# Kernel optimization log

Measured on AMD Instinct MI355X. Metric: run time of the kernel, lower is better.

The kernel has to match this reference:

```python
import jax, jax.numpy as jnp
import numpy as np

B, K, D = 8192, 64, 128
LOW_BOUND = 1
TAU = 1.0  # global_step=None -> tau = 1.0


def setup_inputs() -> dict:
    key = jax.random.key(0)
    ks = jax.random.split(key, 7)
    slots = jax.random.normal(ks[0], (B, K, D), dtype=jnp.float32)
    gumbel_u = jax.random.uniform(ks[1], (B, K, 2), dtype=jnp.float32)
    fix_u = jax.random.uniform(ks[2], (B, K), dtype=jnp.float32)
    # score_net params: Linear(D, D//2) -> ReLU -> Linear(D//2, 2)
    H = D // 2
    W1 = jax.random.normal(ks[3], (D, H), dtype=jnp.float32) / np.sqrt(D)
    b1 = jnp.zeros((H,), dtype=jnp.float32)
    W2 = jax.random.normal(ks[4], (H, 2), dtype=jnp.float32) / np.sqrt(H)
    b2 = jnp.zeros((2,), dtype=jnp.float32)
    return {"slots": slots, "gumbel_u": gumbel_u, "fix_u": fix_u,
            "W1": W1, "b1": b1, "W2": W2, "b2": b2}


def reference(slots, gumbel_u, fix_u, W1, b1, W2, b2):
    # score_net MLP: [B,K,D] -> [B,K,2]
    h = jax.nn.relu(jnp.einsum('bkd,dh->bkh', slots, W1) + b1)
    logits = jnp.einsum('bkh,ht->bkt', h, W2) + b2

    # hard gumbel-softmax (training path), straight-through estimator
    u = jnp.clip(gumbel_u, 1e-10, 1.0 - 1e-7)
    g = -jnp.log(-jnp.log(u))
    y_soft = jax.nn.softmax((logits + g) / TAU, axis=-1)
    y_hard = jax.nn.one_hot(jnp.argmax(y_soft, axis=-1), 2, dtype=y_soft.dtype)
    y = y_hard + y_soft - jax.lax.stop_gradient(y_soft)
    decision = y[..., 1]  # [B, K]

    # vectorized _ensure_minimum_slots: activate `deficit` random inactive slots
    active = decision != 0                                   # [B, K]
    needed = jnp.maximum(LOW_BOUND - active.sum(-1), 0)[:, None]  # [B, 1]
    keys = jnp.where(active, -jnp.inf, fix_u)                # random keys on inactive slots
    ranks = jnp.argsort(jnp.argsort(-keys, axis=-1), axis=-1)  # rank 0 = largest key
    activate = (ranks < needed) & (~active)
    decision = jnp.where(activate, jnp.asarray(1.0, decision.dtype), decision)

    keep_probs = jax.nn.softmax(logits, axis=-1)[..., 1]     # [B, K]
    return decision, keep_probs
```

## Files before the change

### kernel.cpp

```cpp
#include <hip/hip_runtime.h>


typedef __attribute__((ext_vector_type(8))) short bf16x8;
typedef __attribute__((ext_vector_type(4))) float f32x4;

constexpr int NROWS = 8192 * 64;
constexpr int D = 128, H = 64;

__device__ __forceinline__ void split3(float x, unsigned& h1, unsigned& h2, unsigned& h3) {
    unsigned ux = __float_as_uint(x);
    h1 = ux & 0xFFFF0000u;
    float r = x - __uint_as_float(h1);
    h2 = __float_as_uint(r) & 0xFFFF0000u;
    float r2 = r - __uint_as_float(h2);
    h3 = __float_as_uint(r2) & 0xFFFF0000u;
}

__global__ __launch_bounds__(512, 2)
void gumbel_slot_mfma(const float* __restrict__ slots,
                      const float* __restrict__ gumbel_u,
                      const float* __restrict__ fix_u,
                      const float* __restrict__ W1,
                      const float* __restrict__ b1,
                      const float* __restrict__ W2,
                      const float* __restrict__ b2,
                      float* __restrict__ out)
{
    __shared__ __align__(16) unsigned short wt[3 * 64 * 128];
    __shared__ __align__(16) float red[8][16][16][2];

    const int tid  = threadIdx.x;
    const int wv   = tid >> 6;
    const int lane = tid & 63;
    const int quad = lane >> 4;
    const int col  = lane & 15;

#pragma unroll
    for (int i = 0; i < 16; ++i) {
        const int e = i * 512 + tid;
        const int d = e >> 6, j = e & 63;
        unsigned h1, h2, h3;
        split3(W1[e], h1, h2, h3);
        const int chunk = (d >> 3) ^ (j & 15);
        const int idx = j * 128 + chunk * 8 + (d & 7);
        wt[idx]             = (unsigned short)(h1 >> 16);
        wt[idx + 8192]      = (unsigned short)(h2 >> 16);
        wt[idx + 16384]     = (unsigned short)(h3 >> 16);
    }
    __syncthreads();

    float  b1v[4];
    float2 w2v[4];
#pragma unroll
    for (int nt = 0; nt < 4; ++nt) {
        b1v[nt] = b1[nt * 16 + col];
        w2v[nt] = *(const float2*)(W2 + (size_t)(nt * 16 + col) * 2);
    }
    const float2 b2v = *(const float2*)b2;

#pragma unroll 1
    for (int t = 0; t < 2; ++t) {
        const int tile = blockIdx.x + t * 512;
        const int rowW = tile * 512 + wv * 64;
        const int r    = rowW + lane;

        f32x4 acc[4][4];
#pragma unroll
        for (int mt = 0; mt < 4; ++mt)
#pragma unroll
            for (int nt = 0; nt < 4; ++nt)
                acc[mt][nt] = f32x4{b1v[nt], b1v[nt], b1v[nt], b1v[nt]};

#pragma unroll 1
        for (int ks = 0; ks < 4; ++ks) {
            bf16x8 a1[4], a2[4], a3[4];
#pragma unroll
            for (int mt = 0; mt < 4; ++mt) {
                const float* arow = slots + (size_t)(rowW + mt * 16 + col) * D
                                          + ks * 32 + quad * 8;
                const float4 x0 = *(const float4*)arow;
                const float4 x1 = *(const float4*)(arow + 4);
                const float xs[8] = {x0.x, x0.y, x0.z, x0.w, x1.x, x1.y, x1.z, x1.w};
                union { int i[4]; bf16x8 v; } u1, u2, u3;
#pragma unroll
                for (int p = 0; p < 4; ++p) {
                    unsigned xh1, xh2, xh3, yh1, yh2, yh3;
                    split3(xs[2 * p],     xh1, xh2, xh3);
                    split3(xs[2 * p + 1], yh1, yh2, yh3);
                    u1.i[p] = (int)((xh1 >> 16) | yh1);
                    u2.i[p] = (int)((xh2 >> 16) | yh2);
                    u3.i[p] = (int)((xh3 >> 16) | yh3);
                }
                a1[mt] = u1.v; a2[mt] = u2.v; a3[mt] = u3.v;
            }
#pragma unroll
            for (int nt = 0; nt < 4; ++nt) {
                const int j = nt * 16 + col;
                const int chunk = (ks * 4 + quad) ^ col;
                const unsigned short* wp = &wt[j * 128 + chunk * 8];
                const bf16x8 bq1 = *(const bf16x8*)(wp);
                const bf16x8 bq2 = *(const bf16x8*)(wp + 8192);
                const bf16x8 bq3 = *(const bf16x8*)(wp + 16384);
#pragma unroll
                for (int mt = 0; mt < 4; ++mt) {
                    f32x4 c = acc[mt][nt];
                    c = __builtin_amdgcn_mfma_f32_16x16x32_bf16(a1[mt], bq1, c, 0, 0, 0);
                    c = __builtin_amdgcn_mfma_f32_16x16x32_bf16(a2[mt], bq1, c, 0, 0, 0);
                    c = __builtin_amdgcn_mfma_f32_16x16x32_bf16(a1[mt], bq2, c, 0, 0, 0);
                    c = __builtin_amdgcn_mfma_f32_16x16x32_bf16(a2[mt], bq2, c, 0, 0, 0);
                    c = __builtin_amdgcn_mfma_f32_16x16x32_bf16(a1[mt], bq3, c, 0, 0, 0);
                    c = __builtin_amdgcn_mfma_f32_16x16x32_bf16(a3[mt], bq1, c, 0, 0, 0);
                    acc[mt][nt] = c;
                }
            }
        }

        float fl0 = 0.f, fl1 = 0.f;
#pragma unroll 1
        for (int mt = 0; mt < 4; ++mt) {
#pragma unroll
            for (int reg = 0; reg < 4; ++reg) {
                float p0 = 0.f, p1 = 0.f;
#pragma unroll
                for (int nt = 0; nt < 4; ++nt) {
                    const float h = fmaxf(acc[mt][nt][reg], 0.f);
                    p0 = fmaf(h, w2v[nt].x, p0);
                    p1 = fmaf(h, w2v[nt].y, p1);
                }
                const int rl = quad * 4 + reg;
                *(float2*)&red[wv][rl][col ^ rl][0] = make_float2(p0, p1);
            }
            __syncthreads();
            if ((lane >> 4) == mt) {
                const int rl = col;
                float s0 = 0.f, s1 = 0.f;
#pragma unroll
                for (int c = 0; c < 16; ++c) {
                    const float2 v = *(const float2*)&red[wv][rl][c ^ rl][0];
                    s0 += v.x; s1 += v.y;
                }
                fl0 = s0; fl1 = s1;
            }
            __syncthreads();
        }
        const float l0 = fl0 + b2v.x;
        const float l1 = fl1 + b2v.y;

        const float2 u2 = *(const float2*)(gumbel_u + (size_t)r * 2);
        const float lo = 1e-10f, hi = (float)(1.0 - 1e-7);
        const float u0 = fminf(fmaxf(u2.x, lo), hi);
        const float u1 = fminf(fmaxf(u2.y, lo), hi);
        const float g0 = -logf(-logf(u0));
        const float g1 = -logf(-logf(u1));
        float dec = ((l1 + g1) > (l0 + g0)) ? 1.0f : 0.0f;

        const float m  = fmaxf(l0, l1);
        const float e0 = expf(l0 - m), e1 = expf(l1 - m);
        const float keep = e1 / (e0 + e1);

        const unsigned long long act = __ballot(dec != 0.0f);
        if (act == 0ull) {
            float v = fix_u[r];
            int  idx = lane;
#pragma unroll
            for (int off = 32; off > 0; off >>= 1) {
                const float ov  = __shfl_xor(v, off, 64);
                const int  oidx = __shfl_xor(idx, off, 64);
                if (ov > v || (ov == v && oidx < idx)) { v = ov; idx = oidx; }
            }
            if (lane == idx) dec = 1.0f;
        }

        out[r] = dec;
        out[NROWS + r] = keep;
    }
}

extern "C" void kernel_launch(void* const* d_in, const int* in_sizes, int n_in,
                              void* d_out, int out_size, void* d_ws, size_t ws_size,
                              hipStream_t stream)
{
    const float* slots  = (const float*)d_in[0];
    const float* gumbel = (const float*)d_in[1];
    const float* fixu   = (const float*)d_in[2];
    const float* W1     = (const float*)d_in[3];
    const float* b1     = (const float*)d_in[4];
    const float* W2     = (const float*)d_in[5];
    const float* b2     = (const float*)d_in[6];
    float* out = (float*)d_out;

    gumbel_slot_mfma<<<512, 512, 0, stream>>>(
        slots, gumbel, fixu, W1, b1, W2, b2, out);
}
```

Before: 419.3 us.

## Prefetch slot rows across k-steps, shuffle-reduce logits, use smaller blocks

Restructures the MLP kernel so each wave works on 32-row halves with register double-buffered global loads: the next k-slice is fetched while the current one is split and fed to the MFMAs. The shared-memory logit reduction and its block-wide barriers are replaced by intra-wave xor shuffles. Blocks shrink to 256 threads on a 1024-block grid with 3 blocks per CU. The gumbel load moves up front and the b1 bias is added after accumulation. The aim is to hide slots-load latency and drop barrier stalls, at the cost of register pressure and more per-block weight splitting into LDS.

Result: slower. 537.6 us (+28.2%).

```diff
diff --git a/kernel.cpp b/kernel.cpp
--- a/kernel.cpp
+++ b/kernel.cpp
@@ -5,7 +5,8 @@
 typedef __attribute__((ext_vector_type(4))) float f32x4;
 
 constexpr int NROWS = 8192 * 64;
-constexpr int D = 128, H = 64;
+constexpr int D = 128;
+constexpr int GRID = 1024;
 
 __device__ __forceinline__ void split3(float x, unsigned& h1, unsigned& h2, unsigned& h3) {
     unsigned ux = __float_as_uint(x);
@@ -13,10 +14,19 @@
     float r = x - __uint_as_float(h1);
     h2 = __float_as_uint(r) & 0xFFFF0000u;
     float r2 = r - __uint_as_float(h2);
-    h3 = __float_as_uint(r2) & 0xFFFF0000u;
-}
-
-__global__ __launch_bounds__(512, 2)
+    h3 = __float_as_uint(r2);
+}
+
+__device__ __forceinline__ void split_pair(float x, float y, int& o1, int& o2, int& o3) {
+    unsigned x1, x2, x3, y1, y2, y3;
+    split3(x, x1, x2, x3);
+    split3(y, y1, y2, y3);
+    o1 = (int)((x1 >> 16) | (y1 & 0xFFFF0000u));
+    o2 = (int)((x2 >> 16) | (y2 & 0xFFFF0000u));
+    o3 = (int)((x3 >> 16) | (y3 & 0xFFFF0000u));
+}
+
+__global__ __launch_bounds__(256, 3)
 void gumbel_slot_mfma(const float* __restrict__ slots,
                       const float* __restrict__ gumbel_u,
                       const float* __restrict__ fix_u,
@@ -27,7 +37,6 @@
                       float* __restrict__ out)
 {
     __shared__ __align__(16) unsigned short wt[3 * 64 * 128];
-    __shared__ __align__(16) float red[8][16][16][2];
 
     const int tid  = threadIdx.x;
     const int wv   = tid >> 6;
@@ -36,16 +45,16 @@
     const int col  = lane & 15;
 
 #pragma unroll
-    for (int i = 0; i < 16; ++i) {
-        const int e = i * 512 + tid;
+    for (int i = 0; i < 32; ++i) {
+        const int e = i * 256 + tid;
         const int d = e >> 6, j = e & 63;
         unsigned h1, h2, h3;
         split3(W1[e], h1, h2, h3);
         const int chunk = (d >> 3) ^ (j & 15);
         const int idx = j * 128 + chunk * 8 + (d & 7);
-        wt[idx]             = (unsigned short)(h1 >> 16);
-        wt[idx + 8192]      = (unsigned short)(h2 >> 16);
-        wt[idx + 16384]     = (unsigned short)(h3 >> 16);
+        wt[idx]         = (unsigned short)(h1 >> 16);
+        wt[idx + 8192]  = (unsigned short)(h2 >> 16);
+        wt[idx + 16384] = (unsigned short)(h3 >> 16);
     }
     __syncthreads();
 
@@ -60,99 +69,116 @@
 
 #pragma unroll 1
     for (int t = 0; t < 2; ++t) {
-        const int tile = blockIdx.x + t * 512;
-        const int rowW = tile * 512 + wv * 64;
+        const int tile = blockIdx.x + t * GRID;
+        const int rowW = tile * 256 + wv * 64;
         const int r    = rowW + lane;
 
-        f32x4 acc[4][4];
-#pragma unroll
-        for (int mt = 0; mt < 4; ++mt)
-#pragma unroll
-            for (int nt = 0; nt < 4; ++nt)
-                acc[mt][nt] = f32x4{b1v[nt], b1v[nt], b1v[nt], b1v[nt]};
-
-#pragma unroll 1
-        for (int ks = 0; ks < 4; ++ks) {
-            bf16x8 a1[4], a2[4], a3[4];
-#pragma unroll
-            for (int mt = 0; mt < 4; ++mt) {
-                const float* arow = slots + (size_t)(rowW + mt * 16 + col) * D
-                                          + ks * 32 + quad * 8;
-                const float4 x0 = *(const float4*)arow;
-                const float4 x1 = *(const float4*)(arow + 4);
-                const float xs[8] = {x0.x, x0.y, x0.z, x0.w, x1.x, x1.y, x1.z, x1.w};
-                union { int i[4]; bf16x8 v; } u1, u2, u3;
-#pragma unroll
-                for (int p = 0; p < 4; ++p) {
-                    unsigned xh1, xh2, xh3, yh1, yh2, yh3;
-                    split3(xs[2 * p],     xh1, xh2, xh3);
-                    split3(xs[2 * p + 1], yh1, yh2, yh3);
-                    u1.i[p] = (int)((xh1 >> 16) | yh1);
-                    u2.i[p] = (int)((xh2 >> 16) | yh2);
-                    u3.i[p] = (int)((xh3 >> 16) | yh3);
-                }
-                a1[mt] = u1.v; a2[mt] = u2.v; a3[mt] = u3.v;
+        const float2 g2 = *(const float2*)(gumbel_u + (size_t)r * 2);
+
+        const float* __restrict__ arow0 = slots + (size_t)(rowW + col) * D + quad * 8;
+
+        float l0 = 0.f, l1 = 0.f;
+        float4 raw[2][2];
+
+#pragma unroll
+        for (int mh = 0; mh < 2; ++mh) {
+            raw[mh][0] = *(const float4*)(arow0 + mh * 16 * D);
+            raw[mh][1] = *(const float4*)(arow0 + mh * 16 * D + 4);
+        }
+
+#pragma unroll
+        for (int p = 0; p < 2; ++p) {
+            f32x4 acc[2][4];
+#pragma unroll
+            for (int mh = 0; mh < 2; ++mh)
+#pragma unroll
+                for (int nt = 0; nt < 4; ++nt)
+                    acc[mh][nt] = f32x4{0.f, 0.f, 0.f, 0.f};
+
+#pragma unroll
+            for (int ks = 0; ks < 4; ++ks) {
+                bf16x8 a1[2], a2[2], a3[2];
+#pragma unroll
+                for (int mh = 0; mh < 2; ++mh) {
+                    const float xs[8] = {raw[mh][0].x, raw[mh][0].y, raw[mh][0].z, raw[mh][0].w,
+                                         raw[mh][1].x, raw[mh][1].y, raw[mh][1].z, raw[mh][1].w};
+                    union { int i[4]; bf16x8 v; } u1, u2, u3;
+#pragma unroll
+                    for (int q = 0; q < 4; ++q)
+                        split_pair(xs[2 * q], xs[2 * q + 1], u1.i[q], u2.i[q], u3.i[q]);
+                    a1[mh] = u1.v; a2[mh] = u2.v; a3[mh] = u3.v;
+                }
+
+                if (ks < 3) {
+#pragma unroll
+                    for (int mh = 0; mh < 2; ++mh) {
+                        raw[mh][0] = *(const float4*)(arow0 + (p * 32 + mh * 16) * D + (ks + 1) * 32);
+                        raw[mh][1] = *(const float4*)(arow0 + (p * 32 + mh * 16) * D + (ks + 1) * 32 + 4);
+                    }
+                } else if (p == 0) {
+#pragma unroll
+                    for (int mh = 0; mh < 2; ++mh) {
+                        raw[mh][0] = *(const float4*)(arow0 + (32 + mh * 16) * D);
+                        raw[mh][1] = *(const float4*)(arow0 + (32 + mh * 16) * D + 4);
+                    }
+                }
+
+#pragma unroll
+                for (int nt = 0; nt < 4; ++nt) {
+                    const int j = nt * 16 + col;
+                    const int chunk = (ks * 4 + quad) ^ col;
+                    const unsigned short* wp = &wt[j * 128 + chunk * 8];
+                    const bf16x8 bq1 = *(const bf16x8*)(wp);
+                    const bf16x8 bq2 = *(const bf16x8*)(wp + 8192);
+                    const bf16x8 bq3 = *(const bf16x8*)(wp + 16384);
+#pragma unroll
+                    for (int mh = 0; mh < 2; ++mh) {
+                        f32x4 c = acc[mh][nt];
+                        c = __builtin_amdgcn_mfma_f32_16x16x32_bf16(a1[mh], bq1, c, 0, 0, 0);
+                        c = __builtin_amdgcn_mfma_f32_16x16x32_bf16(a2[mh], bq1, c, 0, 0, 0);
+                        c = __builtin_amdgcn_mfma_f32_16x16x32_bf16(a1[mh], bq2, c, 0, 0, 0);
+                        c = __builtin_amdgcn_mfma_f32_16x16x32_bf16(a2[mh], bq2, c, 0, 0, 0);
+                        c = __builtin_amdgcn_mfma_f32_16x16x32_bf16(a1[mh], bq3, c, 0, 0, 0);
+                        c = __builtin_amdgcn_mfma_f32_16x16x32_bf16(a3[mh], bq1, c, 0, 0, 0);
+                        acc[mh][nt] = c;
+                    }
+                }
             }
-#pragma unroll
-            for (int nt = 0; nt < 4; ++nt) {
-                const int j = nt * 16 + col;
-                const int chunk = (ks * 4 + quad) ^ col;
-                const unsigned short* wp = &wt[j * 128 + chunk * 8];
-                const bf16x8 bq1 = *(const bf16x8*)(wp);
-                const bf16x8 bq2 = *(const bf16x8*)(wp + 8192);
-                const bf16x8 bq3 = *(const bf16x8*)(wp + 16384);
-#pragma unroll
-                for (int mt = 0; mt < 4; ++mt) {
-                    f32x4 c = acc[mt][nt];
-                    c = __builtin_amdgcn_mfma_f32_16x16x32_bf16(a1[mt], bq1, c, 0, 0, 0);
-                    c = __builtin_amdgcn_mfma_f32_16x16x32_bf16(a2[mt], bq1, c, 0, 0, 0);
-                    c = __builtin_amdgcn_mfma_f32_16x16x32_bf16(a1[mt], bq2, c, 0, 0, 0);
-                    c = __builtin_amdgcn_mfma_f32_16x16x32_bf16(a2[mt], bq2, c, 0, 0, 0);
-                    c = __builtin_amdgcn_mfma_f32_16x16x32_bf16(a1[mt], bq3, c, 0, 0, 0);
-                    c = __builtin_amdgcn_mfma_f32_16x16x32_bf16(a3[mt], bq1, c, 0, 0, 0);
-                    acc[mt][nt] = c;
+
+#pragma unroll
+            for (int mh = 0; mh < 2; ++mh) {
+#pragma unroll
+                for (int reg = 0; reg < 4; ++reg) {
+                    float p0 = 0.f, p1 = 0.f;
+#pragma unroll
+                    for (int nt = 0; nt < 4; ++nt) {
+                        const float h = fmaxf(acc[mh][nt][reg] + b1v[nt], 0.f);
+                        p0 = fmaf(h, w2v[nt].x, p0);
+                        p1 = fmaf(h, w2v[nt].y, p1);
+                    }
+#pragma unroll
+                    for (int m = 1; m <= 8; m <<= 1) {
+                        p0 += __shfl_xor(p0, m, 64);
+                        p1 += __shfl_xor(p1, m, 64);
+                    }
+                    const int src = (((lane >> 2) & 3) << 4) | (lane & 15);
+                    const float g0 = __shfl(p0, src, 64);
+                    const float g1 = __shfl(p1, src, 64);
+                    if (((lane >> 5) == p) && (((lane >> 4) & 1) == mh) && ((lane & 3) == reg)) {
+                        l0 = g0; l1 = g1;
+                    }
                 }
             }
         }
 
-        float fl0 = 0.f, fl1 = 0.f;
-#pragma unroll 1
-        for (int mt = 0; mt < 4; ++mt) {
-#pragma unroll
-            for (int reg = 0; reg < 4; ++reg) {
-                float p0 = 0.f, p1 = 0.f;
-#pragma unroll
-                for (int nt = 0; nt < 4; ++nt) {
-                    const float h = fmaxf(acc[mt][nt][reg], 0.f);
-                    p0 = fmaf(h, w2v[nt].x, p0);
-                    p1 = fmaf(h, w2v[nt].y, p1);
-                }
-                const int rl = quad * 4 + reg;
-                *(float2*)&red[wv][rl][col ^ rl][0] = make_float2(p0, p1);
-            }
-            __syncthreads();
-            if ((lane >> 4) == mt) {
-                const int rl = col;
-                float s0 = 0.f, s1 = 0.f;
-#pragma unroll
-                for (int c = 0; c < 16; ++c) {
-                    const float2 v = *(const float2*)&red[wv][rl][c ^ rl][0];
-                    s0 += v.x; s1 += v.y;
-                }
-                fl0 = s0; fl1 = s1;
-            }
-            __syncthreads();
-        }
-        const float l0 = fl0 + b2v.x;
-        const float l1 = fl1 + b2v.y;
-
-        const float2 u2 = *(const float2*)(gumbel_u + (size_t)r * 2);
+        l0 += b2v.x; l1 += b2v.y;
+
         const float lo = 1e-10f, hi = (float)(1.0 - 1e-7);
-        const float u0 = fminf(fmaxf(u2.x, lo), hi);
-        const float u1 = fminf(fmaxf(u2.y, lo), hi);
-        const float g0 = -logf(-logf(u0));
-        const float g1 = -logf(-logf(u1));
-        float dec = ((l1 + g1) > (l0 + g0)) ? 1.0f : 0.0f;
+        const float u0 = fminf(fmaxf(g2.x, lo), hi);
+        const float u1 = fminf(fmaxf(g2.y, lo), hi);
+        const float gn0 = -logf(-logf(u0));
+        const float gn1 = -logf(-logf(u1));
+        float dec = ((l1 + gn1) > (l0 + gn0)) ? 1.0f : 0.0f;
 
         const float m  = fmaxf(l0, l1);
         const float e0 = expf(l0 - m), e1 = expf(l1 - m);
@@ -189,6 +215,6 @@
     const float* b2     = (const float*)d_in[6];
     float* out = (float*)d_out;
 
-    gumbel_slot_mfma<<<512, 512, 0, stream>>>(
+    gumbel_slot_mfma<<<GRID, 256, 0, stream>>>(
         slots, gumbel, fixu, W1, b1, W2, b2, out);
 }
```
